# Kernel optimization log

Measured on AMD Instinct MI355X. Metric: run time of the kernel, lower is better.

The kernel has to match this reference:

```python
import jax, jax.numpy as jnp
import numpy as np

NEG = jnp.float32(-1e30)  # finite stand-in for -inf (grad-safe)
BLANK = 0


def setup_inputs() -> dict:
    key = jax.random.key(0)
    k1, k2, k3, k4 = jax.random.split(key, 4)
    B, T, V, S = 64, 1024, 128, 256
    logits = jax.random.normal(k1, (B, T, V), dtype=jnp.float32)
    log_probs = jax.nn.log_softmax(logits, axis=-1)  # valid log-probs like a model head
    log_probs_length = jax.random.randint(k2, (B,), 768, T + 1)
    text_encoded = jax.random.randint(k3, (B, S), 1, V)  # labels exclude blank=0
    text_encoded_length = jax.random.randint(k4, (B,), 64, S + 1)
    return {
        "log_probs": log_probs,
        "log_probs_length": log_probs_length,
        "text_encoded": text_encoded,
        "text_encoded_length": text_encoded_length,
    }


def _ctc_loss(log_probs, input_lengths, targets, target_lengths):
    """CTC loss, matching torch.nn.CTCLoss(blank=0, reduction='mean', zero_infinity=True)."""
    B, T, V = log_probs.shape
    S = targets.shape[1]
    L2 = 2 * S + 1  # extended label sequence: blank-interleaved

    # extended labels ext[b, s]: blank at even s, target[(s-1)//2] at odd s
    ext = jnp.full((B, L2), BLANK, dtype=targets.dtype)
    ext = ext.at[:, 1::2].set(targets)

    # gather per-step log-prob of each extended label: [B, T, L2]
    lp_ext = jnp.take_along_axis(
        log_probs, jnp.broadcast_to(ext[:, None, :], (B, T, L2)), axis=2
    )

    pos = jnp.arange(L2)
    valid_s = pos[None, :] < (2 * target_lengths[:, None] + 1)  # [B, L2]
    ext_m2 = jnp.pad(ext, ((0, 0), (2, 0)), constant_values=BLANK)[:, :-2]
    # skip transition s-2 -> s allowed only at non-blank (odd) positions with differing labels
    skip_mask = (pos[None, :] >= 2) & (pos[None, :] % 2 == 1) & (ext != ext_m2)

    alpha0 = jnp.full((B, L2), NEG, dtype=log_probs.dtype)
    alpha0 = alpha0.at[:, 0].set(lp_ext[:, 0, 0])
    alpha0 = alpha0.at[:, 1].set(jnp.where(target_lengths > 0, lp_ext[:, 0, 1], NEG))
    alpha0 = jnp.where(valid_s, alpha0, NEG)

    lp_ext_T = jnp.moveaxis(lp_ext, 1, 0)  # [T, B, L2]

    def step(alpha, x):
        lp_t, t = x
        s1 = jnp.pad(alpha, ((0, 0), (1, 0)), constant_values=NEG)[:, :-1]
        s2 = jnp.pad(alpha, ((0, 0), (2, 0)), constant_values=NEG)[:, :-2]
        a = jnp.logaddexp(alpha, s1)
        a = jnp.where(skip_mask, jnp.logaddexp(a, s2), a)
        new = jnp.where(valid_s, a + lp_t, NEG)
        # freeze alpha for samples whose input sequence has ended
        new = jnp.where((t < input_lengths)[:, None], new, alpha)
        return new, None

    alpha, _ = jax.lax.scan(step, alpha0, (lp_ext_T[1:], jnp.arange(1, T)))

    L = target_lengths
    idx1 = (2 * L)[:, None]
    idx0 = jnp.maximum(2 * L - 1, 0)[:, None]
    a_blank = jnp.take_along_axis(alpha, idx1, axis=1)[:, 0]
    a_label = jnp.take_along_axis(alpha, idx0, axis=1)[:, 0]
    ll = jnp.logaddexp(a_blank, jnp.where(L > 0, a_label, NEG))
    loss_b = -ll
    # zero_infinity: zero out infeasible alignments
    loss_b = jnp.where(loss_b > 1e29, jnp.float32(0.0), loss_b)
    # reduction='mean': divide each loss by its target length, then batch-mean
    return jnp.mean(loss_b / jnp.maximum(L, 1).astype(log_probs.dtype))


def reference(log_probs, log_probs_length, text_encoded, text_encoded_length):
    return _ctc_loss(log_probs, log_probs_length, text_encoded, text_encoded_length)
```

## Files before the change

kernel.cpp:

```cpp
#include <hip/hip_runtime.h>

constexpr int B_ = 64;
constexpr int T_ = 1024;
constexpr int V_ = 128;
constexpr int S_ = 256;
constexpr int GRING = 32;
constexpr int ROWF = 384;
constexpr int NGW = 3;
constexpr float INV_LN2 = 1.4426950408889634f;
constexpr float LN2 = 0.6931471805599453f;

#define WG_SCOPE __HIP_MEMORY_SCOPE_WORKGROUP

__device__ __forceinline__ void poll_eq(int* p, int want) {
    while (__hip_atomic_load(p, __ATOMIC_RELAXED, WG_SCOPE) != want)
        __builtin_amdgcn_s_sleep(1);
}

__device__ __forceinline__ int wave_rescale(float a[10], int& K) {
    float mx = a[0];
    #pragma unroll
    for (int k = 1; k < 10; ++k) mx = fmaxf(mx, a[k]);
    #pragma unroll
    for (int d = 1; d < 64; d <<= 1) mx = fmaxf(mx, __shfl_xor(mx, d, 64));
    int e;
    (void)frexpf(mx, &e);
    const int ks = (mx > 0.0f) ? (124 - e) : 0;
    #pragma unroll
    for (int k = 0; k < 10; ++k) a[k] = ldexpf(a[k], ks);
    K += ks;
    return ks;
}

__global__ __launch_bounds__(512) void ctc_fused7(
    const float* __restrict__ lp,
    const int* __restrict__ in_len,
    const int* __restrict__ tgt,
    const int* __restrict__ tgt_len,
    float* __restrict__ ws)
{
    const int b    = blockIdx.x;
    const int tid  = threadIdx.x;
    const int wid  = tid >> 6;
    const int lane = tid & 63;

    __shared__ float ringF[GRING * ROWF];
    __shared__ float ringB[GRING * ROWF];
    __shared__ float dumpA[640];
    __shared__ float dumpB[640];
    __shared__ int   tagF[8], tagB[8];
    __shared__ int   consF, consB;
    __shared__ int   KFsh, KBsh;

    const int L  = tgt_len[b];
    const int Tb = in_len[b];
    const float* lpb = lp + (size_t)b * T_ * V_;
    const int* tg = tgt + b * S_;

    const int tm = (Tb - 2) >> 1;
    const int Uf = tm;
    const int Ub = Tb - 2 - tm;

    if (tid == 0) { consF = 0; consB = 0; }
    if (tid < 8) tagF[tid] = -1;
    else if (tid < 16) tagB[tid - 8] = -1;
    __syncthreads();

    if (wid >= 2) {
        const int gw  = wid - 2;
        const int dir = gw / NGW;
        const int q   = gw % NGW;
        const int U   = dir ? Ub : Uf;
        float* ring   = dir ? ringB : ringF;
        int*   tags   = dir ? tagB  : tagF;
        int*   consp  = dir ? &consB : &consF;

        int   perm[5], oddc[5];
        float vmask[5];
        #pragma unroll
        for (int c = 0; c < 5; ++c) {
            const int j = 5 * lane + c;
            if (j < L) { const int lb = tg[j]; perm[c] = lb >> 1; oddc[c] = lb & 1; vmask[c] = 1.0f; }
            else       { perm[c] = 0; oddc[c] = 0; vmask[c] = 0.0f; }
        }

        float2 R0[4], R1[4];
        auto issue = [&](float2 (&Rb)[4], int m) {
            const int n = min(4, U - 4 * m);
            #pragma unroll
            for (int r = 0; r < 4; ++r) {
                if (r < n) {
                    const int u = 4 * m + 1 + r;
                    const int t = dir ? (Tb - 1 - u) : u;
                    Rb[r] = *(const float2*)(lpb + (size_t)t * V_ + 2 * lane);
                }
            }
        };
        auto process = [&](float2 (&Rb)[4], int m) {
            while (__hip_atomic_load(consp, __ATOMIC_RELAXED, WG_SCOPE) < 4 * m - 28)
                __builtin_amdgcn_s_sleep(1);
            const int n = min(4, U - 4 * m);
            #pragma unroll
            for (int r = 0; r < 4; ++r) {
                if (r < n) {
                    const float e0 = __builtin_exp2f(Rb[r].x * INV_LN2);
                    const float e1 = __builtin_exp2f(Rb[r].y * INV_LN2);
                    const float b0 = __shfl(e0, 0, 64);
                    float gv[5];
                    #pragma unroll
                    for (int c = 0; c < 5; ++c) {
                        const float lo = __shfl(e0, perm[c], 64);
                        const float hi = __shfl(e1, perm[c], 64);
                        gv[c] = vmask[c] * (oddc[c] ? hi : lo);
                    }
                    float* rb = ring + ((4 * m + r) & (GRING - 1)) * ROWF;
                    ((float2*)rb)[lane]         = make_float2(b0,    gv[0]);
                    ((float2*)(rb + 128))[lane] = make_float2(gv[1], gv[2]);
                    ((float2*)(rb + 256))[lane] = make_float2(gv[3], gv[4]);
                }
            }
            asm volatile("s_waitcnt lgkmcnt(0)" ::: "memory");
            if (lane == 0)
                __hip_atomic_store(&tags[m & 7], m, __ATOMIC_RELAXED, WG_SCOPE);
        };

        int m = q;
        if (4 * m + 1 <= U) {
            issue(R0, m);
            if (4 * (m + NGW) + 1 <= U) issue(R1, m + NGW);
            while (true) {
                process(R0, m);
                if (4 * (m + 2 * NGW) + 1 <= U) issue(R0, m + 2 * NGW);
                m += NGW;
                if (4 * m + 1 > U) break;
                process(R1, m);
                if (4 * (m + 2 * NGW) + 1 <= U) issue(R1, m + 2 * NGW);
                m += NGW;
                if (4 * m + 1 > U) break;
            }
        }
    } else if (wid == 0) {
        float skipf[5];
        #pragma unroll
        for (int c = 0; c < 5; ++c) {
            const int j = 5 * lane + c;
            skipf[c] = (j >= 1 && j < L && tg[j] != tg[j - 1]) ? 1.0f : 0.0f;
        }
        float a[10];
        #pragma unroll
        for (int k = 0; k < 10; ++k) a[k] = 0.0f;
        {
            const float p00 = __builtin_exp2f(lpb[0] * INV_LN2);
            const float p01 = __builtin_exp2f(lpb[tg[0]] * INV_LN2);
            if (lane == 0) { a[0] = p00; a[1] = p01; }
        }
        float u9n = 0.0f;
        int K = 0;

        float2 S[4][12];
        auto readBlock = [&](int set, int m) {
            const int base = ((4 * m) & (GRING - 1)) * ROWF + 2 * lane;
            #pragma unroll
            for (int r = 0; r < 4; ++r)
                #pragma unroll
                for (int pl = 0; pl < 3; ++pl)
                    S[set][r * 3 + pl] =
                        *(const float2*)&ringF[base + r * ROWF + pl * 128];
        };
        auto rowCore = [&](float2 c0, float2 c1, float2 c2) {
            const float u9 = u9n;
            const float p0 = c0.x;
            a[9] = (a[9] + a[8] + skipf[4] * a[7]) * c2.y;
            const float t9 = __shfl_up(a[9], 1, 64);
            u9n = (lane == 0) ? 0.0f : t9;
            a[8] = (a[8] + a[7]) * p0;
            a[7] = (a[7] + a[6] + skipf[3] * a[5]) * c2.x;
            a[6] = (a[6] + a[5]) * p0;
            a[5] = (a[5] + a[4] + skipf[2] * a[3]) * c1.y;
            a[4] = (a[4] + a[3]) * p0;
            a[3] = (a[3] + a[2] + skipf[1] * a[1]) * c1.x;
            a[2] = (a[2] + a[1]) * p0;
            a[1] = (a[1] + a[0] + skipf[0] * u9) * c0.y;
            a[0] = (a[0] + u9) * p0;
        };
        auto row4 = [&](int set) {
            #pragma unroll
            for (int r = 0; r < 4; ++r)
                rowCore(S[set][r * 3], S[set][r * 3 + 1], S[set][r * 3 + 2]);
        };
        auto body = [&](int m, int setc, int setp) {
            if (4 * (m + 2) + 1 <= Uf) {
                poll_eq(&tagF[(m + 2) & 7], m + 2);
                readBlock(setp, m + 2);
            }
            row4(setc);
            if (lane == 0)
                __hip_atomic_store(&consF, 4 * m + 4, __ATOMIC_RELAXED, WG_SCOPE);
        };

        const int MB4 = (Uf / 4) & ~3;
        poll_eq(&tagF[0], 0); readBlock(0, 0);
        poll_eq(&tagF[1], 1); readBlock(1, 1);
        for (int mb = 0; mb < MB4; mb += 4) {
            body(mb + 0, 0, 2);
            body(mb + 1, 1, 3);
            { const int ks = wave_rescale(a, K); u9n = ldexpf(u9n, ks); }
            body(mb + 2, 2, 0);
            body(mb + 3, 3, 1);
            { const int ks = wave_rescale(a, K); u9n = ldexpf(u9n, ks); }
        }
        #pragma unroll
        for (int r = 0; r < 4; ++r)
            if (4 * MB4 + 1 + r <= Uf)
                rowCore(S[0][r * 3], S[0][r * 3 + 1], S[0][r * 3 + 2]);
        #pragma unroll
        for (int r = 0; r < 4; ++r)
            if (4 * MB4 + 5 + r <= Uf)
                rowCore(S[1][r * 3], S[1][r * 3 + 1], S[1][r * 3 + 2]);
        { const int ks = wave_rescale(a, K); u9n = ldexpf(u9n, ks); }
        for (int u = 4 * MB4 + 9; u <= Uf; ++u) {
            const int bu = (u - 1) >> 2;
            poll_eq(&tagF[bu & 7], bu);
            const int base = ((u - 1) & (GRING - 1)) * ROWF + 2 * lane;
            const float2 c0 = *(const float2*)&ringF[base];
            const float2 c1 = *(const float2*)&ringF[base + 128];
            const float2 c2 = *(const float2*)&ringF[base + 256];
            rowCore(c0, c1, c2);
        }

        #pragma unroll
        for (int k = 0; k < 10; ++k) dumpA[10 * lane + k] = a[k];
        if (lane == 0) {
            KFsh = K;
            __hip_atomic_store(&consF, Uf + 64, __ATOMIC_RELAXED, WG_SCOPE);
        }
    } else {
        float sB[5];
        #pragma unroll
        for (int c = 0; c < 5; ++c) {
            const int j = 5 * lane + c + 1;
            sB[c] = (j < L && tg[j] != tg[j - 1]) ? 1.0f : 0.0f;
        }
        float g[10];
        #pragma unroll
        for (int k = 0; k < 10; ++k) g[k] = 0.0f;
        {
            const float pb = __builtin_exp2f(lpb[(size_t)(Tb - 1) * V_] * INV_LN2);
            const float pl = __builtin_exp2f(lpb[(size_t)(Tb - 1) * V_ + tg[L - 1]] * INV_LN2);
            #pragma unroll
            for (int k = 0; k < 10; ++k) {
                const int s = 10 * lane + k;
                if (s == 2 * L)     g[k] = pb;
                if (s == 2 * L - 1) g[k] = pl;
            }
        }
        float t0 = __shfl_down(g[0], 1, 64), t1 = __shfl_down(g[1], 1, 64);
        float d0n = (lane == 63) ? 0.0f : t0;
        float d1n = (lane == 63) ? 0.0f : t1;
        int K = 0;

        float2 S[4][12];
        auto readBlock = [&](int set, int m) {
            const int base = ((4 * m) & (GRING - 1)) * ROWF + 2 * lane;
            #pragma unroll
            for (int r = 0; r < 4; ++r)
                #pragma unroll
                for (int pl = 0; pl < 3; ++pl)
                    S[set][r * 3 + pl] =
                        *(const float2*)&ringB[base + r * ROWF + pl * 128];
        };
        auto rowCore = [&](float2 c0, float2 c1, float2 c2) {
            const float d0 = d0n, d1 = d1n;
            const float p0 = c0.x;
            g[0] = (g[0] + g[1]) * p0;
            g[1] = (g[1] + g[2] + sB[0] * g[3]) * c0.y;
            const float q0 = __shfl_down(g[0], 1, 64);
            const float q1 = __shfl_down(g[1], 1, 64);
            d0n = (lane == 63) ? 0.0f : q0;
            d1n = (lane == 63) ? 0.0f : q1;
            g[2] = (g[2] + g[3]) * p0;
            g[3] = (g[3] + g[4] + sB[1] * g[5]) * c1.x;
            g[4] = (g[4] + g[5]) * p0;
            g[5] = (g[5] + g[6] + sB[2] * g[7]) * c1.y;
            g[6] = (g[6] + g[7]) * p0;
            g[7] = (g[7] + g[8] + sB[3] * g[9]) * c2.x;
            g[8] = (g[8] + g[9]) * p0;
            g[9] = (g[9] + d0 + sB[4] * d1) * c2.y;
        };
        auto row4 = [&](int set) {
            #pragma unroll
            for (int r = 0; r < 4; ++r)
                rowCore(S[set][r * 3], S[set][r * 3 + 1], S[set][r * 3 + 2]);
        };
        auto body = [&](int m, int setc, int setp) {
            if (4 * (m + 2) + 1 <= Ub) {
                poll_eq(&tagB[(m + 2) & 7], m + 2);
                readBlock(setp, m + 2);
            }
            row4(setc);
            if (lane == 0)
                __hip_atomic_store(&consB, 4 * m + 4, __ATOMIC_RELAXED, WG_SCOPE);
        };

        const int MB4 = (Ub / 4) & ~3;
        poll_eq(&tagB[0], 0); readBlock(0, 0);
        poll_eq(&tagB[1], 1); readBlock(1, 1);
        for (int mb = 0; mb < MB4; mb += 4) {
            body(mb + 0, 0, 2);
            body(mb + 1, 1, 3);
            { const int ks = wave_rescale(g, K);
              d0n = ldexpf(d0n, ks); d1n = ldexpf(d1n, ks); }
            body(mb + 2, 2, 0);
            body(mb + 3, 3, 1);
            { const int ks = wave_rescale(g, K);
              d0n = ldexpf(d0n, ks); d1n = ldexpf(d1n, ks); }
        }
        #pragma unroll
        for (int r = 0; r < 4; ++r)
            if (4 * MB4 + 1 + r <= Ub)
                rowCore(S[0][r * 3], S[0][r * 3 + 1], S[0][r * 3 + 2]);
        #pragma unroll
        for (int r = 0; r < 4; ++r)
            if (4 * MB4 + 5 + r <= Ub)
                rowCore(S[1][r * 3], S[1][r * 3 + 1], S[1][r * 3 + 2]);
        { const int ks = wave_rescale(g, K);
          d0n = ldexpf(d0n, ks); d1n = ldexpf(d1n, ks); }
        for (int u = 4 * MB4 + 9; u <= Ub; ++u) {
            const int bu = (u - 1) >> 2;
            poll_eq(&tagB[bu & 7], bu);
            const int base = ((u - 1) & (GRING - 1)) * ROWF + 2 * lane;
            const float2 c0 = *(const float2*)&ringB[base];
            const float2 c1 = *(const float2*)&ringB[base + 128];
            const float2 c2 = *(const float2*)&ringB[base + 256];
            rowCore(c0, c1, c2);
        }

        {
            const float d0 = d0n, d1 = d1n;
            g[0] = g[0] + g[1];
            g[1] = g[1] + g[2] + sB[0] * g[3];
            g[2] = g[2] + g[3];
            g[3] = g[3] + g[4] + sB[1] * g[5];
            g[4] = g[4] + g[5];
            g[5] = g[5] + g[6] + sB[2] * g[7];
            g[6] = g[6] + g[7];
            g[7] = g[7] + g[8] + sB[3] * g[9];
            g[8] = g[8] + g[9];
            g[9] = g[9] + d0 + sB[4] * d1;
        }
        #pragma unroll
        for (int k = 0; k < 10; ++k) dumpB[10 * lane + k] = g[k];
        if (lane == 0) {
            KBsh = K;
            __hip_atomic_store(&consB, Ub + 64, __ATOMIC_RELAXED, WG_SCOPE);
        }
    }

    __syncthreads();
    if (wid == 0) {
        double sum = 0.0;
        #pragma unroll
        for (int k = 0; k < 10; ++k)
            sum += (double)dumpA[10 * lane + k] * (double)dumpB[10 * lane + k];
        #pragma unroll
        for (int d = 1; d < 64; d <<= 1) sum += __shfl_xor(sum, d, 64);
        if (lane == 0) {
            float loss = 0.0f;
            if (sum > 0.0) {
                const long long ub = __double_as_longlong(sum);
                const int ex = (int)((ub >> 52) & 2047) - 1023;
                const double f = __longlong_as_double(
                    (ub & 0x000FFFFFFFFFFFFFLL) | 0x3FF0000000000000LL);
                const float ll2 = __builtin_log2f((float)f)
                                + (float)(ex - KFsh - KBsh);
                loss = -(ll2 * LN2);
                if (!(loss <= 1e29f)) loss = 0.0f;
            }
            ws[b] = loss / (float)L;
        }
    }
}

__global__ void ctc_reduce_kernel(const float* __restrict__ ws, float* __restrict__ out) {
    float v = ws[threadIdx.x];
    #pragma unroll
    for (int o = 32; o > 0; o >>= 1) v += __shfl_down(v, o);
    if (threadIdx.x == 0) out[0] = v / (float)B_;
}

extern "C" void kernel_launch(void* const* d_in, const int* in_sizes, int n_in,
                              void* d_out, int out_size, void* d_ws, size_t ws_size,
                              hipStream_t stream) {
    const float* lp      = (const float*)d_in[0];
    const int*   in_len  = (const int*)d_in[1];
    const int*   tgt     = (const int*)d_in[2];
    const int*   tgt_len = (const int*)d_in[3];
    float* loss = (float*)d_ws;
    float* out  = (float*)d_out;

    ctc_fused7<<<B_, 512, 0, stream>>>(lp, in_len, tgt, tgt_len, loss);
    ctc_reduce_kernel<<<1, 64, 0, stream>>>(loss, out);
}
```

Before: 140.3 us.

## Split forward and backward CTC scans into separate workgroups with a join kernel

The fused kernel ran both the forward (alpha) and backward (beta) recurrences in one 512-thread workgroup per sample. They now run in separate 256-thread workgroups, 128 in total, each with its own LDS ring and three producer waves. Partial results are written to global workspace and combined by a new join kernel. This spreads the two serial chains over more compute units and halves LDS use per block, at the cost of an extra kernel launch and a global round-trip.

Measured after the change: 139.6 us. No clear change (-0.5%).

```diff
diff --git a/kernel.cpp b/kernel.cpp
--- a/kernel.cpp
+++ b/kernel.cpp
@@ -10,6 +10,10 @@
 constexpr float INV_LN2 = 1.4426950408889634f;
 constexpr float LN2 = 0.6931471805599453f;
 
+#define WS_DUMPF(W, b) ((W) + 64 + (size_t)(b) * 640)
+#define WS_DUMPB(W, b) ((W) + 64 + 64 * 640 + (size_t)(b) * 640)
+#define WS_KARR(W)     ((int*)((W) + 64 + 2 * 64 * 640))
+
 #define WG_SCOPE __HIP_MEMORY_SCOPE_WORKGROUP
 
 __device__ __forceinline__ void poll_eq(int* p, int want) {
@@ -32,25 +36,22 @@
     return ks;
 }
 
-__global__ __launch_bounds__(512) void ctc_fused7(
+__global__ __launch_bounds__(256) void ctc_scan(
     const float* __restrict__ lp,
     const int* __restrict__ in_len,
     const int* __restrict__ tgt,
     const int* __restrict__ tgt_len,
-    float* __restrict__ ws)
+    float* __restrict__ W)
 {
-    const int b    = blockIdx.x;
+    const int b    = blockIdx.x & 63;
+    const int dir  = blockIdx.x >> 6;
     const int tid  = threadIdx.x;
     const int wid  = tid >> 6;
     const int lane = tid & 63;
 
-    __shared__ float ringF[GRING * ROWF];
-    __shared__ float ringB[GRING * ROWF];
-    __shared__ float dumpA[640];
-    __shared__ float dumpB[640];
-    __shared__ int   tagF[8], tagB[8];
-    __shared__ int   consF, consB;
-    __shared__ int   KFsh, KBsh;
+    __shared__ float ring[GRING * ROWF];
+    __shared__ int   tags[8];
+    __shared__ int   cons;
 
     const int L  = tgt_len[b];
     const int Tb = in_len[b];
@@ -60,20 +61,14 @@
     const int tm = (Tb - 2) >> 1;
     const int Uf = tm;
     const int Ub = Tb - 2 - tm;
-
-    if (tid == 0) { consF = 0; consB = 0; }
-    if (tid < 8) tagF[tid] = -1;
-    else if (tid < 16) tagB[tid - 8] = -1;
+    const int U  = dir ? Ub : Uf;
+
+    if (tid == 0) cons = 0;
+    if (tid < 8) tags[tid] = -1;
     __syncthreads();
 
-    if (wid >= 2) {
-        const int gw  = wid - 2;
-        const int dir = gw / NGW;
-        const int q   = gw % NGW;
-        const int U   = dir ? Ub : Uf;
-        float* ring   = dir ? ringB : ringF;
-        int*   tags   = dir ? tagB  : tagF;
-        int*   consp  = dir ? &consB : &consF;
+    if (wid >= 1) {
+        const int q = wid - 1;
 
         int   perm[5], oddc[5];
         float vmask[5];
@@ -97,7 +92,7 @@
             }
         };
         auto process = [&](float2 (&Rb)[4], int m) {
-            while (__hip_atomic_load(consp, __ATOMIC_RELAXED, WG_SCOPE) < 4 * m - 28)
+            while (__hip_atomic_load(&cons, __ATOMIC_RELAXED, WG_SCOPE) < 4 * m - 28)
                 __builtin_amdgcn_s_sleep(1);
             const int n = min(4, U - 4 * m);
             #pragma unroll
@@ -139,7 +134,21 @@
                 if (4 * m + 1 > U) break;
             }
         }
-    } else if (wid == 0) {
+        return;
+    }
+
+    float2 S[4][12];
+    auto readBlock = [&](int set, int m) {
+        const int base = ((4 * m) & (GRING - 1)) * ROWF + 2 * lane;
+        #pragma unroll
+        for (int r = 0; r < 4; ++r)
+            #pragma unroll
+            for (int pl = 0; pl < 3; ++pl)
+                S[set][r * 3 + pl] =
+                    *(const float2*)&ring[base + r * ROWF + pl * 128];
+    };
+
+    if (dir == 0) {
         float skipf[5];
         #pragma unroll
         for (int c = 0; c < 5; ++c) {
@@ -157,16 +166,6 @@
         float u9n = 0.0f;
         int K = 0;
 
-        float2 S[4][12];
-        auto readBlock = [&](int set, int m) {
-            const int base = ((4 * m) & (GRING - 1)) * ROWF + 2 * lane;
-            #pragma unroll
-            for (int r = 0; r < 4; ++r)
-                #pragma unroll
-                for (int pl = 0; pl < 3; ++pl)
-                    S[set][r * 3 + pl] =
-                        *(const float2*)&ringF[base + r * ROWF + pl * 128];
-        };
         auto rowCore = [&](float2 c0, float2 c1, float2 c2) {
             const float u9 = u9n;
             const float p0 = c0.x;
@@ -190,17 +189,17 @@
         };
         auto body = [&](int m, int setc, int setp) {
             if (4 * (m + 2) + 1 <= Uf) {
-                poll_eq(&tagF[(m + 2) & 7], m + 2);
+                poll_eq(&tags[(m + 2) & 7], m + 2);
                 readBlock(setp, m + 2);
             }
             row4(setc);
             if (lane == 0)
-                __hip_atomic_store(&consF, 4 * m + 4, __ATOMIC_RELAXED, WG_SCOPE);
+                __hip_atomic_store(&cons, 4 * m + 4, __ATOMIC_RELAXED, WG_SCOPE);
         };
 
         const int MB4 = (Uf / 4) & ~3;
-        poll_eq(&tagF[0], 0); readBlock(0, 0);
-        poll_eq(&tagF[1], 1); readBlock(1, 1);
+        poll_eq(&tags[0], 0); readBlock(0, 0);
+        poll_eq(&tags[1], 1); readBlock(1, 1);
         for (int mb = 0; mb < MB4; mb += 4) {
             body(mb + 0, 0, 2);
             body(mb + 1, 1, 3);
@@ -220,20 +219,18 @@
         { const int ks = wave_rescale(a, K); u9n = ldexpf(u9n, ks); }
         for (int u = 4 * MB4 + 9; u <= Uf; ++u) {
             const int bu = (u - 1) >> 2;
-            poll_eq(&tagF[bu & 7], bu);
+            poll_eq(&tags[bu & 7], bu);
             const int base = ((u - 1) & (GRING - 1)) * ROWF + 2 * lane;
-            const float2 c0 = *(const float2*)&ringF[base];
-            const float2 c1 = *(const float2*)&ringF[base + 128];
-            const float2 c2 = *(const float2*)&ringF[base + 256];
+            const float2 c0 = *(const float2*)&ring[base];
+            const float2 c1 = *(const float2*)&ring[base + 128];
+            const float2 c2 = *(const float2*)&ring[base + 256];
             rowCore(c0, c1, c2);
         }
 
-        #pragma unroll
-        for (int k = 0; k < 10; ++k) dumpA[10 * lane + k] = a[k];
-        if (lane == 0) {
-            KFsh = K;
-            __hip_atomic_store(&consF, Uf + 64, __ATOMIC_RELAXED, WG_SCOPE);
-        }
+        float* dump = WS_DUMPF(W, b);
+        #pragma unroll
+        for (int k = 0; k < 10; ++k) dump[10 * lane + k] = a[k];
+        if (lane == 0) WS_KARR(W)[b] = K;
     } else {
         float sB[5];
         #pragma unroll
@@ -259,16 +256,6 @@
         float d1n = (lane == 63) ? 0.0f : t1;
         int K = 0;
 
-        float2 S[4][12];
-        auto readBlock = [&](int set, int m) {
-            const int base = ((4 * m) & (GRING - 1)) * ROWF + 2 * lane;
-            #pragma unroll
-            for (int r = 0; r < 4; ++r)
-                #pragma unroll
-                for (int pl = 0; pl < 3; ++pl)
-                    S[set][r * 3 + pl] =
-                        *(const float2*)&ringB[base + r * ROWF + pl * 128];
-        };
         auto rowCore = [&](float2 c0, float2 c1, float2 c2) {
             const float d0 = d0n, d1 = d1n;
             const float p0 = c0.x;
@@ -294,17 +281,17 @@
         };
         auto body = [&](int m, int setc, int setp) {
             if (4 * (m + 2) + 1 <= Ub) {
-                poll_eq(&tagB[(m + 2) & 7], m + 2);
+                poll_eq(&tags[(m + 2) & 7], m + 2);
                 readBlock(setp, m + 2);
             }
             row4(setc);
             if (lane == 0)
-                __hip_atomic_store(&consB, 4 * m + 4, __ATOMIC_RELAXED, WG_SCOPE);
+                __hip_atomic_store(&cons, 4 * m + 4, __ATOMIC_RELAXED, WG_SCOPE);
         };
 
         const int MB4 = (Ub / 4) & ~3;
-        poll_eq(&tagB[0], 0); readBlock(0, 0);
-        poll_eq(&tagB[1], 1); readBlock(1, 1);
+        poll_eq(&tags[0], 0); readBlock(0, 0);
+        poll_eq(&tags[1], 1); readBlock(1, 1);
         for (int mb = 0; mb < MB4; mb += 4) {
             body(mb + 0, 0, 2);
             body(mb + 1, 1, 3);
@@ -327,11 +314,11 @@
           d0n = ldexpf(d0n, ks); d1n = ldexpf(d1n, ks); }
         for (int u = 4 * MB4 + 9; u <= Ub; ++u) {
             const int bu = (u - 1) >> 2;
-            poll_eq(&tagB[bu & 7], bu);
+            poll_eq(&tags[bu & 7], bu);
             const int base = ((u - 1) & (GRING - 1)) * ROWF + 2 * lane;
-            const float2 c0 = *(const float2*)&ringB[base];
-            const float2 c1 = *(const float2*)&ringB[base + 128];
-            const float2 c2 = *(const float2*)&ringB[base + 256];
+            const float2 c0 = *(const float2*)&ring[base];
+            const float2 c1 = *(const float2*)&ring[base + 128];
+            const float2 c2 = *(const float2*)&ring[base + 256];
             rowCore(c0, c1, c2);
         }
 
@@ -348,36 +335,43 @@
             g[8] = g[8] + g[9];
             g[9] = g[9] + d0 + sB[4] * d1;
         }
-        #pragma unroll
-        for (int k = 0; k < 10; ++k) dumpB[10 * lane + k] = g[k];
-        if (lane == 0) {
-            KBsh = K;
-            __hip_atomic_store(&consB, Ub + 64, __ATOMIC_RELAXED, WG_SCOPE);
-        }
+        float* dump = WS_DUMPB(W, b);
+        #pragma unroll
+        for (int k = 0; k < 10; ++k) dump[10 * lane + k] = g[k];
+        if (lane == 0) WS_KARR(W)[64 + b] = K;
     }
-
-    __syncthreads();
-    if (wid == 0) {
-        double sum = 0.0;
-        #pragma unroll
-        for (int k = 0; k < 10; ++k)
-            sum += (double)dumpA[10 * lane + k] * (double)dumpB[10 * lane + k];
-        #pragma unroll
-        for (int d = 1; d < 64; d <<= 1) sum += __shfl_xor(sum, d, 64);
-        if (lane == 0) {
-            float loss = 0.0f;
-            if (sum > 0.0) {
-                const long long ub = __double_as_longlong(sum);
-                const int ex = (int)((ub >> 52) & 2047) - 1023;
-                const double f = __longlong_as_double(
-                    (ub & 0x000FFFFFFFFFFFFFLL) | 0x3FF0000000000000LL);
-                const float ll2 = __builtin_log2f((float)f)
-                                + (float)(ex - KFsh - KBsh);
-                loss = -(ll2 * LN2);
-                if (!(loss <= 1e29f)) loss = 0.0f;
-            }
-            ws[b] = loss / (float)L;
-        }
+}
+
+__global__ void ctc_join_kernel(const float* __restrict__ W_const,
+                                const int* __restrict__ tgt_len,
+                                float* __restrict__ lossArr) {
+    const int b = blockIdx.x;
+    const int lane = threadIdx.x;
+    float* W = const_cast<float*>(W_const);
+    const float* dA = WS_DUMPF(W, b);
+    const float* dB = WS_DUMPB(W, b);
+    double sum = 0.0;
+    #pragma unroll
+    for (int k = 0; k < 10; ++k)
+        sum += (double)dA[10 * lane + k] * (double)dB[10 * lane + k];
+    #pragma unroll
+    for (int d = 1; d < 64; d <<= 1) sum += __shfl_xor(sum, d, 64);
+    if (lane == 0) {
+        const int L = tgt_len[b];
+        const int KF = WS_KARR(W)[b];
+        const int KB = WS_KARR(W)[64 + b];
+        float loss = 0.0f;
+        if (sum > 0.0) {
+            const long long ub = __double_as_longlong(sum);
+            const int ex = (int)((ub >> 52) & 2047) - 1023;
+            const double f = __longlong_as_double(
+                (ub & 0x000FFFFFFFFFFFFFLL) | 0x3FF0000000000000LL);
+            const float ll2 = __builtin_log2f((float)f)
+                            + (float)(ex - KF - KB);
+            loss = -(ll2 * LN2);
+            if (!(loss <= 1e29f)) loss = 0.0f;
+        }
+        lossArr[b] = loss / (float)L;
     }
 }
 
@@ -395,9 +389,10 @@
     const int*   in_len  = (const int*)d_in[1];
     const int*   tgt     = (const int*)d_in[2];
     const int*   tgt_len = (const int*)d_in[3];
-    float* loss = (float*)d_ws;
-    float* out  = (float*)d_out;
-
-    ctc_fused7<<<B_, 512, 0, stream>>>(lp, in_len, tgt, tgt_len, loss);
-    ctc_reduce_kernel<<<1, 64, 0, stream>>>(loss, out);
-}
+    float* W   = (float*)d_ws;
+    float* out = (float*)d_out;
+
+    ctc_scan<<<2 * B_, 256, 0, stream>>>(lp, in_len, tgt, tgt_len, W);
+    ctc_join_kernel<<<B_, 64, 0, stream>>>(W, tgt_len, W);
+    ctc_reduce_kernel<<<1, 64, 0, stream>>>(W, out);
+}
```
